# Performance work log

Hardware: AMD Instinct MI355X
Metric: run time of the kernel (lower is better)

The kernel has to match this reference:

```python
import jax, jax.numpy as jnp
import numpy as np

B, D_IN, T = 16, 512, 4096
D_CB, K = 8, 1024
COMMITMENT = 1.0


def _weight_norm(v, g):
    # torch weight_norm with dim=0: w[o] = g[o] * v[o] / ||v[o]||
    return g[:, None] * v / jnp.sqrt(jnp.sum(v * v, axis=1, keepdims=True))


def setup_inputs() -> dict:
    key = jax.random.key(0)
    ks = jax.random.split(key, 8)
    return {
        "z": jax.random.normal(ks[0], (B, D_IN, T), dtype=jnp.float32),
        "in_v": jax.random.normal(ks[1], (D_CB, D_IN), dtype=jnp.float32) * 0.05,
        "in_g": jax.random.uniform(ks[2], (D_CB,), dtype=jnp.float32, minval=0.5, maxval=1.5),
        "in_b": jax.random.normal(ks[3], (D_CB,), dtype=jnp.float32) * 0.01,
        "out_v": jax.random.normal(ks[4], (D_IN, D_CB), dtype=jnp.float32) * 0.05,
        "out_g": jax.random.uniform(ks[5], (D_IN,), dtype=jnp.float32, minval=0.5, maxval=1.5),
        "out_b": jax.random.normal(ks[6], (D_IN,), dtype=jnp.float32) * 0.01,
        "codebook": jax.random.normal(ks[7], (K, D_CB), dtype=jnp.float32),
    }


def reference(z, in_v, in_g, in_b, out_v, out_g, out_b, codebook):
    z = z.astype(jnp.float32)
    # in_project: weight-normed 1x1 conv == per-timestep linear [D_IN -> D_CB]
    w_in = _weight_norm(in_v, in_g)                       # [D_CB, D_IN]
    z_e = jnp.einsum('cd,bdt->bct', w_in, z) + in_b[None, :, None]  # [B, D_CB, T]

    enc = jnp.transpose(z_e, (0, 2, 1))                   # [B, T, D_CB]
    cb = codebook.astype(jnp.float32)                     # [K, D_CB]
    # squared euclidean distance via expansion
    d = (jnp.sum(enc * enc, axis=-1, keepdims=True)
         - 2.0 * jnp.einsum('btd,kd->btk', enc, cb)
         + jnp.sum(cb * cb, axis=-1)[None, None, :])      # [B, T, K]
    indices = jnp.argmin(d, axis=-1)                      # [B, T] int

    z_q = jnp.transpose(cb[indices], (0, 2, 1))           # [B, D_CB, T]
    commit_loss = jnp.mean((z_e - jax.lax.stop_gradient(z_q)) ** 2, axis=(1, 2)) * COMMITMENT  # [B]

    # straight-through estimator
    z_q_st = z_e + jax.lax.stop_gradient(z_q - z_e)

    w_out = _weight_norm(out_v, out_g)                    # [D_IN, D_CB]
    out = jnp.einsum('cd,bdt->bct', w_out, z_q_st) + out_b[None, :, None]  # [B, D_IN, T]
    return out, commit_loss, indices
```

## Files before the change

### kernel.cpp

```cpp
#include <hip/hip_runtime.h>
#include <math.h>

#define NB 16
#define DIN 512
#define TT 4096
#define DCB 8
#define KC 1024
#define NW 8
#define TC 128


__global__ __launch_bounds__(512) void vq_setup(
    const float* __restrict__ in_v, const float* __restrict__ in_g,
    const float* __restrict__ out_v, const float* __restrict__ out_g,
    const float* __restrict__ cb, float* __restrict__ ws)
{
    int tid = threadIdx.x;
    float* w_inT = ws;
    float* w_out = ws + 4096;
    float* cb2   = ws + 8192;

    {
        int c    = tid >> 6;
        int lane = tid & 63;
        const float* v = in_v + c * DIN;
        float s = 0.f;
        #pragma unroll
        for (int i = 0; i < DIN; i += 64) {
            float x = v[i + lane];
            s += x * x;
        }
        #pragma unroll
        for (int off = 32; off > 0; off >>= 1) s += __shfl_xor(s, off, 64);
        float sq = sqrtf(s);
        float g  = in_g[c];
        #pragma unroll
        for (int i = 0; i < DIN; i += 64) {
            int d = i + lane;
            w_inT[d * DCB + c] = (g * v[d]) / sq;
        }
    }
    {
        int o = tid;
        const float* v = out_v + o * DCB;
        float s = 0.f;
        #pragma unroll
        for (int c = 0; c < DCB; ++c) s += v[c] * v[c];
        float sq = sqrtf(s);
        float g  = out_g[o];
        #pragma unroll
        for (int c = 0; c < DCB; ++c) w_out[o * DCB + c] = (g * v[c]) / sq;
    }
    for (int k = tid; k < KC; k += 512) {
        const float* r = cb + k * DCB;
        float s = 0.f;
        #pragma unroll
        for (int c = 0; c < DCB; ++c) s += r[c] * r[c];
        cb2[k] = s;
    }
}

__global__ __launch_bounds__(512, 4) void vq_main(
    const float* __restrict__ z, const float* __restrict__ in_b,
    const float* __restrict__ out_b, const float* __restrict__ cb,
    const float* __restrict__ ws, float* __restrict__ ws_commit,
    float* __restrict__ out)
{
    const float* w_inT = ws;
    const float* w_out = ws + 4096;
    const float* cb2   = ws + 8192;

    __shared__ float red[NW][DCB][TC];
    __shared__ float sd[NW][TC];
    __shared__ int   si[NW][TC];
    __shared__ float scl[NW];

    int w    = threadIdx.x >> 6;
    int wu   = __builtin_amdgcn_readfirstlane(w);
    int lane = threadIdx.x & 63;
    int blk  = blockIdx.x;
    int b    = blk >> 5;
    int t0   = (blk & 31) * TC;
    int tl   = 2 * lane;

    const float* zp = z + (size_t)b * DIN * TT + t0 + tl;

    float ze0[DCB], ze1[DCB];
    #pragma unroll
    for (int c = 0; c < DCB; ++c) { ze0[c] = 0.f; ze1[c] = 0.f; }

    int d0 = wu * 64;
    #pragma unroll 4
    for (int dd = 0; dd < 64; ++dd) {
        int d = d0 + dd;
        float2 zv = *(const float2*)(zp + (size_t)d * TT);
        const float* wi = w_inT + d * DCB;
        #pragma unroll
        for (int c = 0; c < DCB; ++c) {
            ze0[c] = fmaf(wi[c], zv.x, ze0[c]);
            ze1[c] = fmaf(wi[c], zv.y, ze1[c]);
        }
    }

    #pragma unroll
    for (int c = 0; c < DCB; ++c) {
        red[w][c][tl]     = ze0[c];
        red[w][c][tl + 1] = ze1[c];
    }
    __syncthreads();
    #pragma unroll
    for (int c = 0; c < DCB; ++c) {
        float s0 = 0.f, s1 = 0.f;
        #pragma unroll
        for (int w2 = 0; w2 < NW; ++w2) {
            s0 += red[w2][c][tl];
            s1 += red[w2][c][tl + 1];
        }
        ze0[c] = s0 + in_b[c];
        ze1[c] = s1 + in_b[c];
    }

    float enc20 = 0.f, enc21 = 0.f;
    #pragma unroll
    for (int c = 0; c < DCB; ++c) {
        enc20 += ze0[c] * ze0[c];
        enc21 += ze1[c] * ze1[c];
    }

    float best0 = 3.4e38f, best1 = 3.4e38f;
    int   bi0   = 0,       bi1   = 0;
    int   k0    = wu * 128;
    #pragma unroll 4
    for (int kk = 0; kk < 128; ++kk) {
        int k = k0 + kk;
        const float* r = cb + k * DCB;
        float dot0 = 0.f, dot1 = 0.f;
        #pragma unroll
        for (int c = 0; c < DCB; ++c) {
            dot0 = fmaf(ze0[c], r[c], dot0);
            dot1 = fmaf(ze1[c], r[c], dot1);
        }
        float c2 = cb2[k];
        float dk0 = (enc20 - 2.0f * dot0) + c2;
        float dk1 = (enc21 - 2.0f * dot1) + c2;
        if (dk0 < best0) { best0 = dk0; bi0 = k; }
        if (dk1 < best1) { best1 = dk1; bi1 = k; }
    }
    sd[w][tl]     = best0;  si[w][tl]     = bi0;
    sd[w][tl + 1] = best1;  si[w][tl + 1] = bi1;
    __syncthreads();

    float g0 = sd[0][tl], g1 = sd[0][tl + 1];
    int  gi0 = si[0][tl], gi1 = si[0][tl + 1];
    #pragma unroll
    for (int w2 = 1; w2 < NW; ++w2) {
        float d0_ = sd[w2][tl],     d1_ = sd[w2][tl + 1];
        int   i0_ = si[w2][tl],     i1_ = si[w2][tl + 1];
        if (d0_ < g0) { g0 = d0_; gi0 = i0_; }
        if (d1_ < g1) { g1 = d1_; gi1 = i1_; }
    }

    const float* cq0 = cb + (size_t)gi0 * DCB;
    const float* cq1 = cb + (size_t)gi1 * DCB;
    float zst0[DCB], zst1[DCB];
    float cl = 0.f;
    #pragma unroll
    for (int c = 0; c < DCB; ++c) {
        float q0 = cq0[c], q1 = cq1[c];
        float f0 = ze0[c] - q0, f1 = ze1[c] - q1;
        cl = fmaf(f0, f0, cl);
        cl = fmaf(f1, f1, cl);
        zst0[c] = ze0[c] + (q0 - ze0[c]);
        zst1[c] = ze1[c] + (q1 - ze1[c]);
    }
    #pragma unroll
    for (int off = 32; off > 0; off >>= 1) cl += __shfl_xor(cl, off, 64);
    if (lane == 0) scl[w] = cl;

    if (wu == 0) {
        float2 iv = make_float2((float)gi0, (float)gi1);
        *(float2*)(out + (size_t)NB * DIN * TT + NB + (size_t)b * TT + t0 + tl) = iv;
    }

    float* outp = out + (size_t)b * DIN * TT + t0 + tl;
    int o0 = wu * 64;
    #pragma unroll 4
    for (int oo = 0; oo < 64; ++oo) {
        int o = o0 + oo;
        const float* wo = w_out + o * DCB;
        float a0 = 0.f, a1 = 0.f;
        #pragma unroll
        for (int c = 0; c < DCB; ++c) {
            a0 = fmaf(wo[c], zst0[c], a0);
            a1 = fmaf(wo[c], zst1[c], a1);
        }
        float ob = out_b[o];
        *(float2*)(outp + (size_t)o * TT) = make_float2(a0 + ob, a1 + ob);
    }

    __syncthreads();
    if (threadIdx.x == 0) {
        float s = 0.f;
        #pragma unroll
        for (int w2 = 0; w2 < NW; ++w2) s += scl[w2];
        ws_commit[blk] = s;
    }
}

__global__ __launch_bounds__(64) void vq_commit(
    const float* __restrict__ ws_commit, float* __restrict__ out)
{
    int b    = blockIdx.x;
    int lane = threadIdx.x;
    float s = (lane < 32) ? ws_commit[b * 32 + lane] : 0.f;
    #pragma unroll
    for (int off = 32; off > 0; off >>= 1) s += __shfl_xor(s, off, 64);
    if (lane == 0)
        out[(size_t)NB * DIN * TT + b] = s * (1.0f / (DCB * TT));
}

extern "C" void kernel_launch(void* const* d_in, const int* in_sizes, int n_in,
                              void* d_out, int out_size, void* d_ws, size_t ws_size,
                              hipStream_t stream) {
    const float* z     = (const float*)d_in[0];
    const float* in_v  = (const float*)d_in[1];
    const float* in_g  = (const float*)d_in[2];
    const float* in_b  = (const float*)d_in[3];
    const float* out_v = (const float*)d_in[4];
    const float* out_g = (const float*)d_in[5];
    const float* out_b = (const float*)d_in[6];
    const float* cb    = (const float*)d_in[7];

    float* ws  = (float*)d_ws;
    float* out = (float*)d_out;

    vq_setup<<<1, 512, 0, stream>>>(in_v, in_g, out_v, out_g, cb, ws);
    vq_main<<<512, 512, 0, stream>>>(z, in_b, out_b, cb, ws, ws + 9216, out);
    vq_commit<<<NB, 64, 0, stream>>>(ws + 9216, out);
}
```

Baseline: 73.13 us.

## Split fused VQ kernel into partial projection, codebook scan, and output kernels

```diff
diff --git a/kernel.cpp b/kernel.cpp
--- a/kernel.cpp
+++ b/kernel.cpp
@@ -6,8 +6,10 @@
 #define TT 4096
 #define DCB 8
 #define KC 1024
-#define NW 8
-#define TC 128
+#define DQ 4
+#define ZEP_OFF 10240
+#define ZEP_FLOATS (NB * DQ * DCB * TT)
+#define WS_NEED ((size_t)(ZEP_OFF + ZEP_FLOATS) * sizeof(float))
 
 
 __global__ __launch_bounds__(512) void vq_setup(
@@ -60,7 +62,181 @@
     }
 }
 
-__global__ __launch_bounds__(512, 4) void vq_main(
+
+__global__ __launch_bounds__(256) void vq_zepart(
+    const float* __restrict__ z, const float* __restrict__ ws,
+    float* __restrict__ zep)
+{
+    const float* w_inT = ws;
+    int blk = blockIdx.x;
+    int b   = blk >> 5;
+    int dq  = (blk >> 3) & 3;
+    int tc  = blk & 7;
+    int t   = tc * 512 + 2 * threadIdx.x;
+
+    const float* zp = z + (size_t)b * DIN * TT + t;
+
+    float ze0[DCB], ze1[DCB];
+    #pragma unroll
+    for (int c = 0; c < DCB; ++c) { ze0[c] = 0.f; ze1[c] = 0.f; }
+
+    int d0 = dq * 128;
+    #pragma unroll 8
+    for (int dd = 0; dd < 128; ++dd) {
+        int d = d0 + dd;
+        float2 zv = *(const float2*)(zp + (size_t)d * TT);
+        const float* wi = w_inT + d * DCB;
+        #pragma unroll
+        for (int c = 0; c < DCB; ++c) {
+            ze0[c] = fmaf(wi[c], zv.x, ze0[c]);
+            ze1[c] = fmaf(wi[c], zv.y, ze1[c]);
+        }
+    }
+    float* o = zep + ((size_t)(b * DQ + dq) * DCB) * TT + t;
+    #pragma unroll
+    for (int c = 0; c < DCB; ++c)
+        *(float2*)(o + (size_t)c * TT) = make_float2(ze0[c], ze1[c]);
+}
+
+__global__ __launch_bounds__(256) void vq_scan(
+    const float* __restrict__ cb, const float* __restrict__ in_b,
+    const float* __restrict__ ws, float* __restrict__ ws_commit,
+    float* __restrict__ out)
+{
+    const float* cb2 = ws + 8192;
+    const float* zep = ws + ZEP_OFF;
+
+    __shared__ float sd[4][64];
+    __shared__ int   si[4][64];
+
+    int w    = threadIdx.x >> 6;
+    int wu   = __builtin_amdgcn_readfirstlane(w);
+    int lane = threadIdx.x & 63;
+    int blk  = blockIdx.x;
+    int b    = blk >> 6;
+    int t    = (blk & 63) * 64 + lane;
+
+    float ze[DCB];
+    #pragma unroll
+    for (int c = 0; c < DCB; ++c) ze[c] = 0.f;
+    #pragma unroll
+    for (int dq = 0; dq < DQ; ++dq) {
+        const float* p = zep + ((size_t)(b * DQ + dq) * DCB) * TT + t;
+        #pragma unroll
+        for (int c = 0; c < DCB; ++c) ze[c] += p[(size_t)c * TT];
+    }
+    #pragma unroll
+    for (int c = 0; c < DCB; ++c) ze[c] += in_b[c];
+
+    float enc2 = 0.f;
+    #pragma unroll
+    for (int c = 0; c < DCB; ++c) enc2 += ze[c] * ze[c];
+
+    float best = 3.4e38f;
+    int   bi   = 0;
+    int   k0   = wu * 256;
+    #pragma unroll 4
+    for (int kk = 0; kk < 256; ++kk) {
+        int k = k0 + kk;
+        const float* r = cb + k * DCB;
+        float dot = 0.f;
+        #pragma unroll
+        for (int c = 0; c < DCB; ++c) dot = fmaf(ze[c], r[c], dot);
+        float dk = (enc2 - 2.0f * dot) + cb2[k];
+        if (dk < best) { best = dk; bi = k; }
+    }
+    sd[w][lane] = best;
+    si[w][lane] = bi;
+    __syncthreads();
+
+    float gbest = sd[0][lane];
+    int   gbi   = si[0][lane];
+    #pragma unroll
+    for (int w2 = 1; w2 < 4; ++w2) {
+        float d2 = sd[w2][lane];
+        int   i2 = si[w2][lane];
+        if (d2 < gbest) { gbest = d2; gbi = i2; }
+    }
+
+    if (wu == 0) {
+        const float* cq = cb + (size_t)gbi * DCB;
+        float cl = 0.f;
+        #pragma unroll
+        for (int c = 0; c < DCB; ++c) {
+            float diff = ze[c] - cq[c];
+            cl = fmaf(diff, diff, cl);
+        }
+        #pragma unroll
+        for (int off = 32; off > 0; off >>= 1) cl += __shfl_xor(cl, off, 64);
+        if (lane == 0) ws_commit[blk] = cl;
+        out[(size_t)NB * DIN * TT + NB + (size_t)b * TT + t] = (float)gbi;
+    }
+}
+
+__global__ __launch_bounds__(256) void vq_out(
+    const float* __restrict__ cb, const float* __restrict__ out_b,
+    const float* __restrict__ ws, float* __restrict__ out)
+{
+    const float* w_out = ws + 4096;
+    const float* idxf  = out + (size_t)NB * DIN * TT + NB;
+
+    int blk  = blockIdx.x;
+    int b    = blk >> 6;
+    int rest = blk & 63;
+    int o0   = (rest >> 4) * 128;
+    int t0   = (rest & 15) * 256;
+    int w    = threadIdx.x >> 6;
+    int wu   = __builtin_amdgcn_readfirstlane(w);
+    int lane = threadIdx.x & 63;
+    int t    = t0 + 4 * lane;
+
+    float4 iv = *(const float4*)(idxf + (size_t)b * TT + t);
+    int k0 = (int)iv.x, k1 = (int)iv.y, k2 = (int)iv.z, k3 = (int)iv.w;
+
+    float4 qa0 = ((const float4*)(cb))[2 * k0], qb0 = ((const float4*)(cb))[2 * k0 + 1];
+    float4 qa1 = ((const float4*)(cb))[2 * k1], qb1 = ((const float4*)(cb))[2 * k1 + 1];
+    float4 qa2 = ((const float4*)(cb))[2 * k2], qb2 = ((const float4*)(cb))[2 * k2 + 1];
+    float4 qa3 = ((const float4*)(cb))[2 * k3], qb3 = ((const float4*)(cb))[2 * k3 + 1];
+
+    int ob = o0 + wu * 32;
+    float* outp = out + (size_t)b * DIN * TT + t;
+
+    #pragma unroll 4
+    for (int oo = 0; oo < 32; ++oo) {
+        int o = ob + oo;
+        const float* wo = w_out + o * DCB;
+        float obias = out_b[o];
+        float a0, a1, a2, a3;
+        a0 = fmaf(wo[0], qa0.x, fmaf(wo[1], qa0.y, fmaf(wo[2], qa0.z, fmaf(wo[3], qa0.w,
+             fmaf(wo[4], qb0.x, fmaf(wo[5], qb0.y, fmaf(wo[6], qb0.z, wo[7] * qb0.w)))))));
+        a1 = fmaf(wo[0], qa1.x, fmaf(wo[1], qa1.y, fmaf(wo[2], qa1.z, fmaf(wo[3], qa1.w,
+             fmaf(wo[4], qb1.x, fmaf(wo[5], qb1.y, fmaf(wo[6], qb1.z, wo[7] * qb1.w)))))));
+        a2 = fmaf(wo[0], qa2.x, fmaf(wo[1], qa2.y, fmaf(wo[2], qa2.z, fmaf(wo[3], qa2.w,
+             fmaf(wo[4], qb2.x, fmaf(wo[5], qb2.y, fmaf(wo[6], qb2.z, wo[7] * qb2.w)))))));
+        a3 = fmaf(wo[0], qa3.x, fmaf(wo[1], qa3.y, fmaf(wo[2], qa3.z, fmaf(wo[3], qa3.w,
+             fmaf(wo[4], qb3.x, fmaf(wo[5], qb3.y, fmaf(wo[6], qb3.z, wo[7] * qb3.w)))))));
+        float4 r = make_float4(a0 + obias, a1 + obias, a2 + obias, a3 + obias);
+        *(float4*)(outp + (size_t)o * TT) = r;
+    }
+}
+
+__global__ __launch_bounds__(64) void vq_commit(
+    const float* __restrict__ ws_commit, float* __restrict__ out)
+{
+    int b    = blockIdx.x;
+    int lane = threadIdx.x;
+    float s = ws_commit[b * 64 + lane];
+    #pragma unroll
+    for (int off = 32; off > 0; off >>= 1) s += __shfl_xor(s, off, 64);
+    if (lane == 0)
+        out[(size_t)NB * DIN * TT + b] = s * (1.0f / (DCB * TT));
+}
+
+
+#define NWF 8
+#define TCF 128
+
+__global__ __launch_bounds__(512, 4) void vq_main_fb(
     const float* __restrict__ z, const float* __restrict__ in_b,
     const float* __restrict__ out_b, const float* __restrict__ cb,
     const float* __restrict__ ws, float* __restrict__ ws_commit,
@@ -70,17 +246,17 @@
     const float* w_out = ws + 4096;
     const float* cb2   = ws + 8192;
 
-    __shared__ float red[NW][DCB][TC];
-    __shared__ float sd[NW][TC];
-    __shared__ int   si[NW][TC];
-    __shared__ float scl[NW];
+    __shared__ float red[NWF][DCB][TCF];
+    __shared__ float sd[NWF][TCF];
+    __shared__ int   si[NWF][TCF];
+    __shared__ float scl[NWF];
 
     int w    = threadIdx.x >> 6;
     int wu   = __builtin_amdgcn_readfirstlane(w);
     int lane = threadIdx.x & 63;
     int blk  = blockIdx.x;
     int b    = blk >> 5;
-    int t0   = (blk & 31) * TC;
+    int t0   = (blk & 31) * TCF;
     int tl   = 2 * lane;
 
     const float* zp = z + (size_t)b * DIN * TT + t0 + tl;
@@ -101,7 +277,6 @@
             ze1[c] = fmaf(wi[c], zv.y, ze1[c]);
         }
     }
-
     #pragma unroll
     for (int c = 0; c < DCB; ++c) {
         red[w][c][tl]     = ze0[c];
@@ -112,7 +287,7 @@
     for (int c = 0; c < DCB; ++c) {
         float s0 = 0.f, s1 = 0.f;
         #pragma unroll
-        for (int w2 = 0; w2 < NW; ++w2) {
+        for (int w2 = 0; w2 < NWF; ++w2) {
             s0 += red[w2][c][tl];
             s1 += red[w2][c][tl + 1];
         }
@@ -153,7 +328,7 @@
     float g0 = sd[0][tl], g1 = sd[0][tl + 1];
     int  gi0 = si[0][tl], gi1 = si[0][tl + 1];
     #pragma unroll
-    for (int w2 = 1; w2 < NW; ++w2) {
+    for (int w2 = 1; w2 < NWF; ++w2) {
         float d0_ = sd[w2][tl],     d1_ = sd[w2][tl + 1];
         int   i0_ = si[w2][tl],     i1_ = si[w2][tl + 1];
         if (d0_ < g0) { g0 = d0_; gi0 = i0_; }
@@ -202,12 +377,12 @@
     if (threadIdx.x == 0) {
         float s = 0.f;
         #pragma unroll
-        for (int w2 = 0; w2 < NW; ++w2) s += scl[w2];
+        for (int w2 = 0; w2 < NWF; ++w2) s += scl[w2];
         ws_commit[blk] = s;
     }
 }
 
-__global__ __launch_bounds__(64) void vq_commit(
+__global__ __launch_bounds__(64) void vq_commit_fb(
     const float* __restrict__ ws_commit, float* __restrict__ out)
 {
     int b    = blockIdx.x;
@@ -235,6 +410,14 @@
     float* out = (float*)d_out;
 
     vq_setup<<<1, 512, 0, stream>>>(in_v, in_g, out_v, out_g, cb, ws);
-    vq_main<<<512, 512, 0, stream>>>(z, in_b, out_b, cb, ws, ws + 9216, out);
-    vq_commit<<<NB, 64, 0, stream>>>(ws + 9216, out);
-}
+
+    if (ws_size >= WS_NEED) {
+        vq_zepart<<<512, 256, 0, stream>>>(z, ws, ws + ZEP_OFF);
+        vq_scan<<<1024, 256, 0, stream>>>(cb, in_b, ws, ws + 9216, out);
+        vq_out<<<1024, 256, 0, stream>>>(cb, out_b, ws, out);
+        vq_commit<<<NB, 64, 0, stream>>>(ws + 9216, out);
+    } else {
+        vq_main_fb<<<512, 512, 0, stream>>>(z, in_b, out_b, cb, ws, ws + 9216, out);
+        vq_commit_fb<<<NB, 64, 0, stream>>>(ws + 9216, out);
+    }
+}
```

Measured after the change: 125.6 us. 1.72x slower.

## Stage codebook and output weights in LDS, compute commit loss in one wave

Applied to the files above, without the earlier changes.

```diff
diff --git a/kernel.cpp b/kernel.cpp
--- a/kernel.cpp
+++ b/kernel.cpp
@@ -66,22 +66,33 @@
     const float* __restrict__ ws, float* __restrict__ ws_commit,
     float* __restrict__ out)
 {
+    __shared__ float s_cb[KC * DCB];
+    __shared__ float s_cb2[KC];
+    __shared__ float s_red[NW * DCB * TC];
+    __shared__ float s_sd[NW][TC];
+    __shared__ int   s_si[NW][TC];
+
     const float* w_inT = ws;
-    const float* w_out = ws + 4096;
-    const float* cb2   = ws + 8192;
-
-    __shared__ float red[NW][DCB][TC];
-    __shared__ float sd[NW][TC];
-    __shared__ int   si[NW][TC];
-    __shared__ float scl[NW];
-
-    int w    = threadIdx.x >> 6;
+
+    int tid  = threadIdx.x;
+    int w    = tid >> 6;
     int wu   = __builtin_amdgcn_readfirstlane(w);
-    int lane = threadIdx.x & 63;
+    int lane = tid & 63;
     int blk  = blockIdx.x;
     int b    = blk >> 5;
     int t0   = (blk & 31) * TC;
     int tl   = 2 * lane;
+
+    float4 cbs0 = ((const float4*)cb)[tid];
+    float4 cbs1 = ((const float4*)cb)[512 + tid];
+    float4 cbs2 = ((const float4*)cb)[1024 + tid];
+    float4 cbs3 = ((const float4*)cb)[1536 + tid];
+    float4 cb2s = make_float4(0.f, 0.f, 0.f, 0.f);
+    if (tid < 256) cb2s = ((const float4*)(ws + 8192))[tid];
+    float4 wos0 = ((const float4*)(ws + 4096))[tid];
+    float4 wos1 = ((const float4*)(ws + 4096))[512 + tid];
+    float4 obs  = make_float4(0.f, 0.f, 0.f, 0.f);
+    if (tid < 128) obs = ((const float4*)out_b)[tid];
 
     const float* zp = z + (size_t)b * DIN * TT + t0 + tl;
 
@@ -102,23 +113,38 @@
         }
     }
 
+    ((float4*)s_cb)[tid]        = cbs0;
+    ((float4*)s_cb)[512 + tid]  = cbs1;
+    ((float4*)s_cb)[1024 + tid] = cbs2;
+    ((float4*)s_cb)[1536 + tid] = cbs3;
+    if (tid < 256) ((float4*)s_cb2)[tid] = cb2s;
+
+    float* redw = s_red + w * DCB * TC;
     #pragma unroll
     for (int c = 0; c < DCB; ++c) {
-        red[w][c][tl]     = ze0[c];
-        red[w][c][tl + 1] = ze1[c];
+        redw[c * TC + tl]     = ze0[c];
+        redw[c * TC + tl + 1] = ze1[c];
     }
     __syncthreads();
+
     #pragma unroll
     for (int c = 0; c < DCB; ++c) {
         float s0 = 0.f, s1 = 0.f;
         #pragma unroll
         for (int w2 = 0; w2 < NW; ++w2) {
-            s0 += red[w2][c][tl];
-            s1 += red[w2][c][tl + 1];
+            s0 += s_red[(w2 * DCB + c) * TC + tl];
+            s1 += s_red[(w2 * DCB + c) * TC + tl + 1];
         }
         ze0[c] = s0 + in_b[c];
         ze1[c] = s1 + in_b[c];
     }
+    __syncthreads();
+
+    float* s_wout = s_red;
+    float* s_outb = s_red + DIN * DCB;
+    ((float4*)s_wout)[tid]       = wos0;
+    ((float4*)s_wout)[512 + tid] = wos1;
+    if (tid < 128) ((float4*)s_outb)[tid] = obs;
 
     float enc20 = 0.f, enc21 = 0.f;
     #pragma unroll
@@ -133,51 +159,49 @@
     #pragma unroll 4
     for (int kk = 0; kk < 128; ++kk) {
         int k = k0 + kk;
-        const float* r = cb + k * DCB;
-        float dot0 = 0.f, dot1 = 0.f;
-        #pragma unroll
-        for (int c = 0; c < DCB; ++c) {
-            dot0 = fmaf(ze0[c], r[c], dot0);
-            dot1 = fmaf(ze1[c], r[c], dot1);
-        }
-        float c2 = cb2[k];
+        float4 r0 = ((const float4*)s_cb)[2 * k];
+        float4 r1 = ((const float4*)s_cb)[2 * k + 1];
+        float dot0 = fmaf(ze0[0], r0.x, fmaf(ze0[1], r0.y, fmaf(ze0[2], r0.z, fmaf(ze0[3], r0.w,
+                     fmaf(ze0[4], r1.x, fmaf(ze0[5], r1.y, fmaf(ze0[6], r1.z, ze0[7] * r1.w)))))));
+        float dot1 = fmaf(ze1[0], r0.x, fmaf(ze1[1], r0.y, fmaf(ze1[2], r0.z, fmaf(ze1[3], r0.w,
+                     fmaf(ze1[4], r1.x, fmaf(ze1[5], r1.y, fmaf(ze1[6], r1.z, ze1[7] * r1.w)))))));
+        float c2  = s_cb2[k];
         float dk0 = (enc20 - 2.0f * dot0) + c2;
         float dk1 = (enc21 - 2.0f * dot1) + c2;
         if (dk0 < best0) { best0 = dk0; bi0 = k; }
         if (dk1 < best1) { best1 = dk1; bi1 = k; }
     }
-    sd[w][tl]     = best0;  si[w][tl]     = bi0;
-    sd[w][tl + 1] = best1;  si[w][tl + 1] = bi1;
+    s_sd[w][tl]     = best0;  s_si[w][tl]     = bi0;
+    s_sd[w][tl + 1] = best1;  s_si[w][tl + 1] = bi1;
     __syncthreads();
 
-    float g0 = sd[0][tl], g1 = sd[0][tl + 1];
-    int  gi0 = si[0][tl], gi1 = si[0][tl + 1];
+    float g0 = s_sd[0][tl], g1 = s_sd[0][tl + 1];
+    int  gi0 = s_si[0][tl], gi1 = s_si[0][tl + 1];
     #pragma unroll
     for (int w2 = 1; w2 < NW; ++w2) {
-        float d0_ = sd[w2][tl],     d1_ = sd[w2][tl + 1];
-        int   i0_ = si[w2][tl],     i1_ = si[w2][tl + 1];
+        float d0_ = s_sd[w2][tl],     d1_ = s_sd[w2][tl + 1];
+        int   i0_ = s_si[w2][tl],     i1_ = s_si[w2][tl + 1];
         if (d0_ < g0) { g0 = d0_; gi0 = i0_; }
         if (d1_ < g1) { g1 = d1_; gi1 = i1_; }
     }
 
-    const float* cq0 = cb + (size_t)gi0 * DCB;
-    const float* cq1 = cb + (size_t)gi1 * DCB;
-    float zst0[DCB], zst1[DCB];
-    float cl = 0.f;
-    #pragma unroll
-    for (int c = 0; c < DCB; ++c) {
-        float q0 = cq0[c], q1 = cq1[c];
-        float f0 = ze0[c] - q0, f1 = ze1[c] - q1;
-        cl = fmaf(f0, f0, cl);
-        cl = fmaf(f1, f1, cl);
-        zst0[c] = ze0[c] + (q0 - ze0[c]);
-        zst1[c] = ze1[c] + (q1 - ze1[c]);
-    }
-    #pragma unroll
-    for (int off = 32; off > 0; off >>= 1) cl += __shfl_xor(cl, off, 64);
-    if (lane == 0) scl[w] = cl;
+    float4 q0a = ((const float4*)s_cb)[2 * gi0], q0b = ((const float4*)s_cb)[2 * gi0 + 1];
+    float4 q1a = ((const float4*)s_cb)[2 * gi1], q1b = ((const float4*)s_cb)[2 * gi1 + 1];
 
     if (wu == 0) {
+        float cl = 0.f;
+        float f;
+        f = ze0[0]-q0a.x; cl = fmaf(f,f,cl);  f = ze1[0]-q1a.x; cl = fmaf(f,f,cl);
+        f = ze0[1]-q0a.y; cl = fmaf(f,f,cl);  f = ze1[1]-q1a.y; cl = fmaf(f,f,cl);
+        f = ze0[2]-q0a.z; cl = fmaf(f,f,cl);  f = ze1[2]-q1a.z; cl = fmaf(f,f,cl);
+        f = ze0[3]-q0a.w; cl = fmaf(f,f,cl);  f = ze1[3]-q1a.w; cl = fmaf(f,f,cl);
+        f = ze0[4]-q0b.x; cl = fmaf(f,f,cl);  f = ze1[4]-q1b.x; cl = fmaf(f,f,cl);
+        f = ze0[5]-q0b.y; cl = fmaf(f,f,cl);  f = ze1[5]-q1b.y; cl = fmaf(f,f,cl);
+        f = ze0[6]-q0b.z; cl = fmaf(f,f,cl);  f = ze1[6]-q1b.z; cl = fmaf(f,f,cl);
+        f = ze0[7]-q0b.w; cl = fmaf(f,f,cl);  f = ze1[7]-q1b.w; cl = fmaf(f,f,cl);
+        #pragma unroll
+        for (int off = 32; off > 0; off >>= 1) cl += __shfl_xor(cl, off, 64);
+        if (lane == 0) ws_commit[blk] = cl;
         float2 iv = make_float2((float)gi0, (float)gi1);
         *(float2*)(out + (size_t)NB * DIN * TT + NB + (size_t)b * TT + t0 + tl) = iv;
     }
@@ -187,23 +211,14 @@
     #pragma unroll 4
     for (int oo = 0; oo < 64; ++oo) {
         int o = o0 + oo;
-        const float* wo = w_out + o * DCB;
-        float a0 = 0.f, a1 = 0.f;
-        #pragma unroll
-        for (int c = 0; c < DCB; ++c) {
-            a0 = fmaf(wo[c], zst0[c], a0);
-            a1 = fmaf(wo[c], zst1[c], a1);
-        }
-        float ob = out_b[o];
-        *(float2*)(outp + (size_t)o * TT) = make_float2(a0 + ob, a1 + ob);
-    }
-
-    __syncthreads();
-    if (threadIdx.x == 0) {
-        float s = 0.f;
-        #pragma unroll
-        for (int w2 = 0; w2 < NW; ++w2) s += scl[w2];
-        ws_commit[blk] = s;
+        float4 wa = ((const float4*)s_wout)[2 * o];
+        float4 wb = ((const float4*)s_wout)[2 * o + 1];
+        float obias = s_outb[o];
+        float a0 = fmaf(wa.x, q0a.x, fmaf(wa.y, q0a.y, fmaf(wa.z, q0a.z, fmaf(wa.w, q0a.w,
+                   fmaf(wb.x, q0b.x, fmaf(wb.y, q0b.y, fmaf(wb.z, q0b.z, wb.w * q0b.w)))))));
+        float a1 = fmaf(wa.x, q1a.x, fmaf(wa.y, q1a.y, fmaf(wa.z, q1a.z, fmaf(wa.w, q1a.w,
+                   fmaf(wb.x, q1b.x, fmaf(wb.y, q1b.y, fmaf(wb.z, q1b.z, wb.w * q1b.w)))))));
+        *(float2*)(outp + (size_t)o * TT) = make_float2(a0 + obias, a1 + obias);
     }
 }
 
```

Measured after the change: 77.67 us. 1.06x slower.
